# Kernel tuning notes

Measured on AMD Instinct MI355X. Metric: run time of the kernel, lower is better.

## Reference

```python
import jax, jax.numpy as jnp
import numpy as np

N = 16384          # input points
IN_PLANES = 64
OUT_PLANES = 128
STRIDE = 4
NSAMPLE = 16
M = N // STRIDE    # sampled points
EPS = 1e-5         # BatchNorm eps


def setup_inputs() -> dict:
    key = jax.random.key(0)
    k1, k2, k3 = jax.random.split(key, 3)
    p = jax.random.uniform(k1, (N, 3), dtype=jnp.float32) * 10.0   # xyz coords
    x = jax.random.normal(k2, (N, IN_PLANES), dtype=jnp.float32)
    o = jnp.array([N], dtype=jnp.int32)                            # single-batch offsets
    W = jax.random.normal(k3, (OUT_PLANES, 3 + IN_PLANES), dtype=jnp.float32) / np.sqrt(3 + IN_PLANES)
    gamma = jnp.ones((OUT_PLANES,), dtype=jnp.float32)
    beta = jnp.zeros((OUT_PLANES,), dtype=jnp.float32)
    return {"p": p, "x": x, "o": o, "W": W, "gamma": gamma, "beta": beta}


def _fps(p, m):
    """Furthest point sampling, starting from point 0 (matches pointops)."""
    n = p.shape[0]

    def step(carry, _):
        dist, last = carry
        d = jnp.sum((p - p[last]) ** 2, axis=1)       # (N,)
        dist = jnp.minimum(dist, d)
        nxt = jnp.argmax(dist).astype(jnp.int32)
        return (dist, nxt), nxt

    init = (jnp.full((n,), 1e10, dtype=jnp.float32), jnp.int32(0))
    _, idxs = jax.lax.scan(step, init, None, length=m - 1)
    return jnp.concatenate([jnp.zeros((1,), jnp.int32), idxs])


def _transition_down(p, x, W, gamma, beta):
    idx = _fps(p, M)
    n_p = p[idx]                                                    # (M,3)
    # kNN query: squared distances (M,N), take NSAMPLE nearest
    d2 = (jnp.sum(n_p ** 2, axis=1, keepdims=True)
          + jnp.sum(p ** 2, axis=1)[None, :]
          - 2.0 * n_p @ p.T)
    _, knn = jax.lax.top_k(-d2, NSAMPLE)                            # (M,NSAMPLE)
    rel = p[knn] - n_p[:, None, :]                                  # grouped relative xyz (M,S,3)
    feats = jnp.concatenate([rel, x[knn]], axis=-1)                 # (M,S,3+C) use_xyz=True
    y = jnp.einsum('msc,oc->mso', feats, W)                         # linear, no bias (M,S,O)
    # BatchNorm1d (training mode): normalize over batch (M) and length (S) dims
    mean = jnp.mean(y, axis=(0, 1))
    var = jnp.var(y, axis=(0, 1))
    y = (y - mean) * jax.lax.rsqrt(var + EPS) * gamma + beta
    y = jax.nn.relu(y)
    y = jnp.max(y, axis=1)                                          # MaxPool1d over nsample -> (M,O)
    return n_p, y


def reference(p, x, o, W, gamma, beta):
    n_p, y = _transition_down(p, x, W, gamma, beta)
    n_o = (o // STRIDE).astype(jnp.int32)
    return (n_p, y, n_o)
```

## Files before the change

kernel.cpp:

```cpp
#include <hip/hip_runtime.h>

#define N_PTS   16384
#define M_PTS   4096
#define NS      16
#define C_IN    64
#define C_FEAT  67
#define C_OUT   128
#define QPB     8
#define GEMM_BLOCKS (M_PTS / QPB)
#define N_O_POS (M_PTS*3 + M_PTS*C_OUT)

#define FPS_T   1024
#define PPT     16

__device__ __forceinline__ unsigned spread3(unsigned x)
{
    x = (x | (x << 16)) & 0x030000FFu;
    x = (x | (x << 8))  & 0x0300F00Fu;
    x = (x | (x << 4))  & 0x030C30C3u;
    x = (x | (x << 2))  & 0x09249249u;
    return x;
}

__global__ __launch_bounds__(1024)
void morton_sort_kernel(const float* __restrict__ p, unsigned* __restrict__ keys)
{
    __shared__ unsigned k_lds[N_PTS];
    const int t = threadIdx.x;
#pragma unroll
    for (int s = 0; s < 16; ++s) {
        const int i = t + (s << 10);
        const float xx = p[3*i+0], yy = p[3*i+1], zz = p[3*i+2];
        unsigned cx = (unsigned)fminf(fmaxf(xx * 6.4f, 0.f), 63.f);
        unsigned cy = (unsigned)fminf(fmaxf(yy * 6.4f, 0.f), 63.f);
        unsigned cz = (unsigned)fminf(fmaxf(zz * 6.4f, 0.f), 63.f);
        const unsigned code = spread3(cx) | (spread3(cy) << 1) | (spread3(cz) << 2);
        k_lds[i] = (code << 14) | (unsigned)i;
    }
    __syncthreads();
    for (unsigned kk = 2; kk <= (unsigned)N_PTS; kk <<= 1) {
        for (unsigned jj = kk >> 1; jj >= 1; jj >>= 1) {
            for (int s = 0; s < 16; ++s) {
                const int i = t + (s << 10);
                const int ixj = i ^ (int)jj;
                if (ixj > i) {
                    const unsigned a = k_lds[i], b = k_lds[ixj];
                    const bool up = ((i & kk) == 0);
                    if (up ? (a > b) : (a < b)) { k_lds[i] = b; k_lds[ixj] = a; }
                }
            }
            __syncthreads();
        }
    }
#pragma unroll
    for (int s = 0; s < 16; ++s) {
        const int i = t + (s << 10);
        keys[i] = k_lds[i];
    }
}

__attribute__((amdgpu_waves_per_eu(4, 4)))
__global__ __launch_bounds__(FPS_T)
void fps_kernel(const float* __restrict__ p, const unsigned* __restrict__ keys,
                int* __restrict__ fidx)
{
#pragma clang fp contract(off)
    const int t    = threadIdx.x;
    const int lane = t & 63;
    const int wid  = t >> 6;

    float px[PPT], py[PPT], pz[PPT], dist[PPT];
    int   oi[PPT];
    float lox =  3e38f, loy =  3e38f, loz =  3e38f;
    float hix = -3e38f, hiy = -3e38f, hiz = -3e38f;

#pragma unroll
    for (int k = 0; k < PPT; ++k) {
        const unsigned key = keys[t * PPT + k];
        const int j = (int)(key & 16383u);
        oi[k] = j;
        px[k] = p[3*j+0]; py[k] = p[3*j+1]; pz[k] = p[3*j+2];
        dist[k] = 1e10f;
        lox = fminf(lox, px[k]); hix = fmaxf(hix, px[k]);
        loy = fminf(loy, py[k]); hiy = fmaxf(hiy, py[k]);
        loz = fminf(loz, pz[k]); hiz = fmaxf(hiz, pz[k]);
    }

    __shared__ float  swv[16];
    __shared__ int    swi[16];
    __shared__ float4 sqv;

    if (t == 0) fidx[0] = 0;
#pragma unroll
    for (int k = 0; k < PPT; ++k)
        if (oi[k] == 0) sqv = make_float4(px[k], py[k], pz[k], 0.f);

    float mymax = 1e10f;  int myidx = -1;

    __syncthreads();

    for (int it = 1; it < M_PTS; ++it) {
        const float4 q4 = sqv;
        const float qx = q4.x, qy = q4.y, qz = q4.z;

        const float gx = fmaxf(fmaxf(lox - qx, qx - hix), 0.f);
        const float gy = fmaxf(fmaxf(loy - qy, qy - hiy), 0.f);
        const float gz = fmaxf(fmaxf(loz - qz, qz - hiz), 0.f);
        const float dlow = (gx*gx + gy*gy + gz*gz) * 0.99999f;

        const bool doflush = (dlow < mymax);
        if (doflush) {
            float bv = -1.f; int bi = 0x7fffffff;
#pragma unroll
            for (int k = 0; k < PPT; ++k) {
                const float dx = px[k] - qx;
                const float dy = py[k] - qy;
                const float dz = pz[k] - qz;
                float d = dx*dx + dy*dy;
                d = d + dz*dz;
                const float nd = fminf(dist[k], d);
                dist[k] = nd;
                const bool tk = (nd > bv) || (nd == bv && oi[k] < bi);
                bv = tk ? nd : bv;  bi = tk ? oi[k] : bi;
            }
            mymax = bv; myidx = bi;
        }
        if (__ballot(doflush)) {
            float v = mymax; int ii = myidx;
#pragma unroll
            for (int off = 1; off < 64; off <<= 1) {
                const float ov = __shfl_xor(v, off, 64);
                const int   oo = __shfl_xor(ii, off, 64);
                const bool tk = (ov > v) || (ov == v && oo < ii);
                v = tk ? ov : v;  ii = tk ? oo : ii;
            }
            if (lane == 0) { swv[wid] = v; swi[wid] = ii; }
        }
        __syncthreads();

        float v2 = swv[lane & 15];  int i2 = swi[lane & 15];
#pragma unroll
        for (int off = 1; off < 16; off <<= 1) {
            const float ov = __shfl_xor(v2, off, 64);
            const int   oo = __shfl_xor(i2, off, 64);
            const bool tk = (ov > v2) || (ov == v2 && oo < i2);
            v2 = tk ? ov : v2;  i2 = tk ? oo : i2;
        }

        if (myidx == i2) {
            float ax = 0.f, ay = 0.f, az = 0.f;
#pragma unroll
            for (int k = 0; k < PPT; ++k) {
                const bool h = (oi[k] == i2);
                ax = h ? px[k] : ax; ay = h ? py[k] : ay; az = h ? pz[k] : az;
            }
            sqv = make_float4(ax, ay, az, 0.f);
            fidx[it] = i2;
            mymax = 3e38f;
        }
        __syncthreads();
    }
}

__global__ __launch_bounds__(256)
void knn_kernel(const float* __restrict__ p, const int* __restrict__ fidx,
                int* __restrict__ knn_out, float* __restrict__ out_np)
{
    const int lane = threadIdx.x & 63;
    const int wid  = threadIdx.x >> 6;
    const int m    = blockIdx.x * 4 + wid;

    const int iq = fidx[m];
    const float qx = p[3*iq+0], qy = p[3*iq+1], qz = p[3*iq+2];
    if (lane == 0) { out_np[m*3+0] = qx; out_np[m*3+1] = qy; out_np[m*3+2] = qz; }

    float d16[16]; int i16[16];
#pragma unroll
    for (int jj = 0; jj < 16; ++jj) {
        const int j = jj*64 + lane;
        const float dx = p[3*j+0]-qx, dy = p[3*j+1]-qy, dz = p[3*j+2]-qz;
        d16[jj] = fmaf(dx, dx, fmaf(dy, dy, dz*dz));
        i16[jj] = j;
    }
    float wv = d16[0];
#pragma unroll
    for (int k = 1; k < 16; ++k) wv = fmaxf(wv, d16[k]);

    for (int jj = 16; jj < 256; ++jj) {
        const int j = jj*64 + lane;
        const float dx = p[3*j+0]-qx, dy = p[3*j+1]-qy, dz = p[3*j+2]-qz;
        const float d = fmaf(dx, dx, fmaf(dy, dy, dz*dz));
        if (d < wv) {
            bool done = false;
#pragma unroll
            for (int k = 0; k < 16; ++k) {
                const bool is = (!done) && (d16[k] == wv);
                d16[k] = is ? d : d16[k];
                i16[k] = is ? j : i16[k];
                done = done || is;
            }
            wv = d16[0];
#pragma unroll
            for (int k = 1; k < 16; ++k) wv = fmaxf(wv, d16[k]);
        }
    }

    float lmv; int lmi;
    {
        lmv = d16[0]; lmi = i16[0];
#pragma unroll
        for (int k = 1; k < 16; ++k) {
            const bool tk = (d16[k] < lmv) || (d16[k] == lmv && i16[k] < lmi);
            lmv = tk ? d16[k] : lmv;  lmi = tk ? i16[k] : lmi;
        }
    }
    int mykn = 0;
    for (int r = 0; r < 16; ++r) {
        float v = lmv; int ii = lmi;
#pragma unroll
        for (int off = 1; off < 64; off <<= 1) {
            const float ov = __shfl_xor(v, off, 64);
            const int   oo = __shfl_xor(ii, off, 64);
            const bool tk = (ov < v) || (ov == v && oo < ii);
            v = tk ? ov : v;  ii = tk ? oo : ii;
        }
        if (lane == r) mykn = ii;
        if (lmi == ii) {
#pragma unroll
            for (int k = 0; k < 16; ++k)
                d16[k] = (i16[k] == ii) ? 3.4e38f : d16[k];
            lmv = d16[0]; lmi = i16[0];
#pragma unroll
            for (int k = 1; k < 16; ++k) {
                const bool tk = (d16[k] < lmv) || (d16[k] == lmv && i16[k] < lmi);
                lmv = tk ? d16[k] : lmv;  lmi = tk ? i16[k] : lmi;
            }
        }
    }
    if (lane < 16) knn_out[m*16 + lane] = mykn;
}

template <int PHASE>
__global__ __launch_bounds__(256)
void gemm_kernel(const float* __restrict__ p, const float* __restrict__ x,
                 const int* __restrict__ knn, const float* __restrict__ W,
                 const float* __restrict__ np_buf, float* __restrict__ part,
                 const float* __restrict__ scsh, float* __restrict__ out_y)
{
    __shared__ float w_lds[C_OUT * C_FEAT];
    __shared__ float feats[NS * 68];
    __shared__ float tmp[512];

    const int tid = threadIdx.x;
    for (int e = tid; e < C_OUT * C_FEAT; e += 256) w_lds[e] = W[e];
    __syncthreads();

    const int o  = tid & 127;
    const int s0 = (tid >> 7) * 8;
    float wreg[C_FEAT];
#pragma unroll
    for (int c = 0; c < C_FEAT; ++c) wreg[c] = w_lds[o * C_FEAT + c];

    float sc = 0.f, sh = 0.f;
    if (PHASE == 1) { sc = scsh[o]; sh = scsh[128 + o]; }

    float lsum = 0.f, lsq = 0.f;

    for (int ml = 0; ml < QPB; ++ml) {
        const int m = blockIdx.x * QPB + ml;
        __syncthreads();
        for (int e = tid; e < NS * C_FEAT; e += 256) {
            const int s = e / C_FEAT;
            const int c = e - s * C_FEAT;
            const int j = knn[m * NS + s];
            float v;
            if (c < 3) v = p[3*j + c] - np_buf[m*3 + c];
            else       v = x[j * C_IN + (c - 3)];
            feats[s * 68 + c] = v;
        }
        __syncthreads();

        float mx = 0.0f;
#pragma unroll
        for (int s8 = 0; s8 < 8; ++s8) {
            const int s = s0 + s8;
            const float4* fr = (const float4*)&feats[s * 68];
            float a = 0.f;
#pragma unroll
            for (int c4 = 0; c4 < 16; ++c4) {
                const float4 f = fr[c4];
                a = fmaf(f.x, wreg[c4*4+0], a);
                a = fmaf(f.y, wreg[c4*4+1], a);
                a = fmaf(f.z, wreg[c4*4+2], a);
                a = fmaf(f.w, wreg[c4*4+3], a);
            }
            a = fmaf(feats[s*68+64], wreg[64], a);
            a = fmaf(feats[s*68+65], wreg[65], a);
            a = fmaf(feats[s*68+66], wreg[66], a);
            if (PHASE == 0) { lsum += a; lsq = fmaf(a, a, lsq); }
            else {
                float v = fmaf(a, sc, sh);
                v = fmaxf(v, 0.f);
                mx = fmaxf(mx, v);
            }
        }
        if (PHASE == 1) {
            tmp[tid] = mx;
            __syncthreads();
            if (tid < 128) out_y[m * C_OUT + o] = fmaxf(tmp[tid], tmp[tid + 128]);
        }
    }

    if (PHASE == 0) {
        tmp[tid] = lsum; tmp[256 + tid] = lsq;
        __syncthreads();
        if (tid < 128) {
            part[blockIdx.x * 256 + o]       = tmp[tid] + tmp[tid + 128];
            part[blockIdx.x * 256 + 128 + o] = tmp[256 + tid] + tmp[256 + tid + 128];
        }
    }
}

__global__ __launch_bounds__(128)
void stats_kernel(const float* __restrict__ part, const float* __restrict__ gamma,
                  const float* __restrict__ beta, float* __restrict__ scsh,
                  float* __restrict__ out)
{
    const int o = threadIdx.x;
    float s = 0.f, s2 = 0.f;
    for (int b = 0; b < GEMM_BLOCKS; ++b) {
        s  += part[b * 256 + o];
        s2 += part[b * 256 + 128 + o];
    }
    const float inv  = 1.0f / 65536.0f;
    const float mean = s * inv;
    const float var  = fmaf(s2, inv, -mean * mean);
    const float sc   = gamma[o] * rsqrtf(var + 1e-5f);
    const float sh   = fmaf(-mean, sc, beta[o]);
    scsh[o] = sc; scsh[128 + o] = sh;
    if (o == 0) out[N_O_POS] = 4096.0f;
}

extern "C" void kernel_launch(void* const* d_in, const int* in_sizes, int n_in,
                              void* d_out, int out_size, void* d_ws, size_t ws_size,
                              hipStream_t stream)
{
    const float* p     = (const float*)d_in[0];
    const float* x     = (const float*)d_in[1];
    const float* W     = (const float*)d_in[3];
    const float* gamma = (const float*)d_in[4];
    const float* beta  = (const float*)d_in[5];
    float* out = (float*)d_out;

    int*      fidx = (int*)d_ws;
    int*      knn  = fidx + M_PTS;
    float*    part = (float*)(knn + M_PTS * NS);
    float*    scsh = part + GEMM_BLOCKS * 256;
    unsigned* keys = (unsigned*)(scsh + 256);

    float* out_np = out;
    float* out_y  = out + M_PTS * 3;

    morton_sort_kernel<<<dim3(1), dim3(1024), 0, stream>>>(p, keys);
    fps_kernel<<<dim3(1), dim3(FPS_T), 0, stream>>>(p, keys, fidx);
    knn_kernel<<<dim3(M_PTS / 4), dim3(256), 0, stream>>>(p, fidx, knn, out_np);
    gemm_kernel<0><<<dim3(GEMM_BLOCKS), dim3(256), 0, stream>>>(
        p, x, knn, W, out_np, part, scsh, out_y);
    stats_kernel<<<dim3(1), dim3(128), 0, stream>>>(part, gamma, beta, scsh, out);
    gemm_kernel<1><<<dim3(GEMM_BLOCKS), dim3(256), 0, stream>>>(
        p, x, knn, W, out_np, part, scsh, out_y);
}
```

Baseline: 11.07 ms.

## Carry winner coordinates through FPS reductions and drop second barrier per iteration

The FPS loop now carries each candidate's xyz through the wave and block argmax shuffles, so every thread learns the next query point directly. This removes the owner-thread write to a shared query slot and the second __syncthreads per iteration, using a double-buffered shared reduction buffer instead. To make room in registers, x/y coordinates move to LDS and the point indices are packed two per register, and the waves-per-EU attribute is removed. In exchange there are more shuffles per reduction step and LDS loads inside the distance update.

After: 11.54 ms. 1.04x slower.

```diff
diff --git a/kernel.cpp b/kernel.cpp
--- a/kernel.cpp
+++ b/kernel.cpp
@@ -59,7 +59,6 @@
     }
 }
 
-__attribute__((amdgpu_waves_per_eu(4, 4)))
 __global__ __launch_bounds__(FPS_T)
 void fps_kernel(const float* __restrict__ p, const unsigned* __restrict__ keys,
                 int* __restrict__ fidx)
@@ -69,40 +68,39 @@
     const int lane = t & 63;
     const int wid  = t >> 6;
 
-    float px[PPT], py[PPT], pz[PPT], dist[PPT];
-    int   oi[PPT];
+    __shared__ float2 pxy[PPT][FPS_T];
+    __shared__ float  swbuf[2][5][16];
+
+    float pz[PPT], dist[PPT];
+    unsigned oi2[PPT/2];
     float lox =  3e38f, loy =  3e38f, loz =  3e38f;
     float hix = -3e38f, hiy = -3e38f, hiz = -3e38f;
 
 #pragma unroll
+    for (int k2 = 0; k2 < PPT/2; ++k2) oi2[k2] = 0u;
+#pragma unroll
     for (int k = 0; k < PPT; ++k) {
         const unsigned key = keys[t * PPT + k];
-        const int j = (int)(key & 16383u);
-        oi[k] = j;
-        px[k] = p[3*j+0]; py[k] = p[3*j+1]; pz[k] = p[3*j+2];
-        dist[k] = 1e10f;
-        lox = fminf(lox, px[k]); hix = fmaxf(hix, px[k]);
-        loy = fminf(loy, py[k]); hiy = fmaxf(hiy, py[k]);
-        loz = fminf(loz, pz[k]); hiz = fmaxf(hiz, pz[k]);
-    }
-
-    __shared__ float  swv[16];
-    __shared__ int    swi[16];
-    __shared__ float4 sqv;
-
+        const unsigned j   = key & 16383u;
+        oi2[k >> 1] |= j << ((k & 1) * 16);
+        const float x = p[3*j+0], y = p[3*j+1], z = p[3*j+2];
+        pxy[k][t] = make_float2(x, y);
+        pz[k] = z;  dist[k] = 1e10f;
+        lox = fminf(lox, x); hix = fmaxf(hix, x);
+        loy = fminf(loy, y); hiy = fmaxf(hiy, y);
+        loz = fminf(loz, z); hiz = fmaxf(hiz, z);
+    }
+    float qx = p[0], qy = p[1], qz = p[2];
     if (t == 0) fidx[0] = 0;
-#pragma unroll
-    for (int k = 0; k < PPT; ++k)
-        if (oi[k] == 0) sqv = make_float4(px[k], py[k], pz[k], 0.f);
 
     float mymax = 1e10f;  int myidx = -1;
+    float mycx = 0.f, mycy = 0.f, mycz = 0.f;
+    float wv = -1.f, wx = 0.f, wy = 0.f, wz = 0.f;  int wi = 0x7fffffff;
+    int par = 0;
 
     __syncthreads();
 
     for (int it = 1; it < M_PTS; ++it) {
-        const float4 q4 = sqv;
-        const float qx = q4.x, qy = q4.y, qz = q4.z;
-
         const float gx = fmaxf(fmaxf(lox - qx, qx - hix), 0.f);
         const float gy = fmaxf(fmaxf(loy - qy, qy - hiy), 0.f);
         const float gz = fmaxf(fmaxf(loz - qz, qz - hiz), 0.f);
@@ -110,55 +108,74 @@
 
         const bool doflush = (dlow < mymax);
         if (doflush) {
-            float bv = -1.f; int bi = 0x7fffffff;
+            float bv = -1.f;  int bi = 0x7fffffff, bk = 0;
 #pragma unroll
             for (int k = 0; k < PPT; ++k) {
-                const float dx = px[k] - qx;
-                const float dy = py[k] - qy;
+                const float2 xy = pxy[k][t];
+                const float dx = xy.x - qx;
+                const float dy = xy.y - qy;
                 const float dz = pz[k] - qz;
                 float d = dx*dx + dy*dy;
                 d = d + dz*dz;
                 const float nd = fminf(dist[k], d);
                 dist[k] = nd;
-                const bool tk = (nd > bv) || (nd == bv && oi[k] < bi);
-                bv = tk ? nd : bv;  bi = tk ? oi[k] : bi;
-            }
-            mymax = bv; myidx = bi;
+                const int oik = (int)((oi2[k >> 1] >> ((k & 1) * 16)) & 0xFFFFu);
+                const bool tk = (nd > bv) || (nd == bv && oik < bi);
+                bv = tk ? nd : bv;  bi = tk ? oik : bi;  bk = tk ? k : bk;
+            }
+            mymax = bv;  myidx = bi;
+            const float2 cxy = pxy[bk][t];
+            mycx = cxy.x;  mycy = cxy.y;
+            float cz = pz[0];
+#pragma unroll
+            for (int k = 1; k < PPT; ++k) cz = (bk == k) ? pz[k] : cz;
+            mycz = cz;
         }
         if (__ballot(doflush)) {
-            float v = mymax; int ii = myidx;
+            float v = mymax, x = mycx, y = mycy, z = mycz;  int ii = myidx;
 #pragma unroll
             for (int off = 1; off < 64; off <<= 1) {
                 const float ov = __shfl_xor(v, off, 64);
                 const int   oo = __shfl_xor(ii, off, 64);
+                const float ox = __shfl_xor(x, off, 64);
+                const float oy = __shfl_xor(y, off, 64);
+                const float oz = __shfl_xor(z, off, 64);
                 const bool tk = (ov > v) || (ov == v && oo < ii);
                 v = tk ? ov : v;  ii = tk ? oo : ii;
-            }
-            if (lane == 0) { swv[wid] = v; swi[wid] = ii; }
+                x = tk ? ox : x;  y  = tk ? oy : y;  z = tk ? oz : z;
+            }
+            wv = v;  wi = ii;  wx = x;  wy = y;  wz = z;
+        }
+        if (lane == 0) {
+            swbuf[par][0][wid] = wv;
+            swbuf[par][1][wid] = __int_as_float(wi);
+            swbuf[par][2][wid] = wx;
+            swbuf[par][3][wid] = wy;
+            swbuf[par][4][wid] = wz;
         }
         __syncthreads();
 
-        float v2 = swv[lane & 15];  int i2 = swi[lane & 15];
+        const int e = lane & 15;
+        float v2 = swbuf[par][0][e];
+        int   i2 = __float_as_int(swbuf[par][1][e]);
+        float x2 = swbuf[par][2][e];
+        float y2 = swbuf[par][3][e];
+        float z2 = swbuf[par][4][e];
 #pragma unroll
         for (int off = 1; off < 16; off <<= 1) {
             const float ov = __shfl_xor(v2, off, 64);
             const int   oo = __shfl_xor(i2, off, 64);
+            const float ox = __shfl_xor(x2, off, 64);
+            const float oy = __shfl_xor(y2, off, 64);
+            const float oz = __shfl_xor(z2, off, 64);
             const bool tk = (ov > v2) || (ov == v2 && oo < i2);
             v2 = tk ? ov : v2;  i2 = tk ? oo : i2;
-        }
-
-        if (myidx == i2) {
-            float ax = 0.f, ay = 0.f, az = 0.f;
-#pragma unroll
-            for (int k = 0; k < PPT; ++k) {
-                const bool h = (oi[k] == i2);
-                ax = h ? px[k] : ax; ay = h ? py[k] : ay; az = h ? pz[k] : az;
-            }
-            sqv = make_float4(ax, ay, az, 0.f);
-            fidx[it] = i2;
-            mymax = 3e38f;
-        }
-        __syncthreads();
+            x2 = tk ? ox : x2;  y2 = tk ? oy : y2;  z2 = tk ? oz : z2;
+        }
+        if (t == 0) fidx[it] = i2;
+        if (myidx == i2) mymax = 3e38f;
+        qx = x2;  qy = y2;  qz = z2;
+        par ^= 1;
     }
 }
 
```
